# Optimization experiments

Hardware: AMD Instinct MI355X
Metric: run time of the kernel (lower is better)

The kernel has to match this reference:

```python
import jax, jax.numpy as jnp
import numpy as np

EMBED_DIM = 2048
NUM_EMBED = 1000
NUM_CLASSES = 1000
BS = 8192


def setup_inputs() -> dict:
    key = jax.random.key(0)
    ks = jax.random.split(key, 9)
    d = EMBED_DIM
    feat = jax.random.normal(ks[0], (BS, d), dtype=jnp.float32)
    # nn.Embedding weight init: uniform(0, 3)
    embeddings = jax.random.uniform(ks[1], (NUM_EMBED, d), dtype=jnp.float32, minval=0.0, maxval=3.0)
    # kaiming normal for square attention matrices
    std = float(np.sqrt(2.0 / d))
    Kw = jax.random.normal(ks[2], (d, d), dtype=jnp.float32) * std
    Qw = jax.random.normal(ks[3], (d, d), dtype=jnp.float32) * std
    Vw = jax.random.normal(ks[4], (d, d), dtype=jnp.float32) * std
    # fc_fuse: Linear(2d -> d); torch default uniform(-1/sqrt(fan_in), 1/sqrt(fan_in))
    b1 = 1.0 / np.sqrt(2 * d)
    fuse_w = jax.random.uniform(ks[5], (d, 2 * d), dtype=jnp.float32, minval=-b1, maxval=b1)
    fuse_b = jax.random.uniform(ks[6], (d,), dtype=jnp.float32, minval=-b1, maxval=b1)
    b2 = 1.0 / np.sqrt(d)
    fc_w = jax.random.uniform(ks[7], (NUM_CLASSES, d), dtype=jnp.float32, minval=-b2, maxval=b2)
    fc_b = jax.random.uniform(ks[8], (NUM_CLASSES,), dtype=jnp.float32, minval=-b2, maxval=b2)
    return {"feat": feat, "embeddings": embeddings, "Kw": Kw, "Qw": Qw, "Vw": Vw,
            "fuse_w": fuse_w, "fuse_b": fuse_b, "fc_w": fc_w, "fc_b": fc_b}


def _l2norm(x, axis=1, eps=1e-12):
    n = jnp.sqrt(jnp.sum(x * x, axis=axis, keepdims=True))
    return x / jnp.maximum(n, eps)


def reference(feat, embeddings, Kw, Qw, Vw, fuse_w, fuse_b, fc_w, fc_b):
    bs = feat.shape[0]
    # --- get_code_indices: normalize rows, pairwise sq-distance, argmin ---
    xn = _l2norm(feat)                       # [bs, d]
    wn = _l2norm(embeddings)                 # [N, d]
    distances = (jnp.sum(xn * xn, axis=1, keepdims=True)
                 + jnp.sum(wn * wn, axis=1)
                 - 2.0 * xn @ wn.T)          # [bs, N]
    idx = jnp.argmin(distances, axis=1)      # [bs]
    # quantize gathers from the UNnormalized table
    quantized = embeddings[idx]              # [bs, d]
    # --- tiny-sequence KQV attention over the 2-token 'sequence' ---
    fuse = jnp.stack([quantized, feat], axis=2)          # [bs, d, 2]
    K = jnp.einsum('ij,bjk->bik', Kw, fuse)              # [bs, d, 2]
    Q = jnp.einsum('ij,bjk->bik', Qw, fuse)              # [bs, d, 2]
    V = jnp.einsum('ij,bjk->bik', Vw, fuse)              # [bs, d, 2]
    scores = jnp.einsum('bdk,bdl->bkl', K, Q)            # K^T Q, [bs, 2, 2]
    # eval-path softmax over dim=1 (no sqrt(2) scaling)
    A = jax.nn.softmax(scores, axis=1)                   # [bs, 2, 2]
    out = jnp.einsum('bdk,bkl->bdl', V, A)               # [bs, d, 2]
    flat = jnp.transpose(out, (0, 2, 1)).reshape(bs, -1) # [bs, 2d]
    h = jax.nn.relu(flat @ fuse_w.T + fuse_b)            # [bs, d]
    pred = h @ fc_w.T + fc_b                             # [bs, num_classes]
    return (quantized, pred, idx)
```

## Files before the change

kernel.cpp:

```cpp
#include <hip/hip_runtime.h>
#include <cstdint>
#include <cstddef>


typedef __bf16 bf16;
typedef __bf16 bf16x8 __attribute__((ext_vector_type(8)));
typedef float  f32x4  __attribute__((ext_vector_type(4)));

#define TO_AS1(p) ((__attribute__((address_space(1))) void*)(uintptr_t)(p))
#define TO_AS3(p) ((__attribute__((address_space(3))) void*)(uintptr_t)(p))

enum { EPI_DIST = 1, EPI_SCORES = 2, EPI_BIAS = 4 };

__device__ __forceinline__ void stage_b(const bf16* __restrict__ src, char* lds,
                                        int rbase, int ld, int k0, int clamp,
                                        int tid) {
  const int wb = tid & ~63, lane = tid & 63;
#pragma unroll
  for (int it = 0; it < 4; ++it) {
    const int chunk = it * 256 + wb + lane;
    const int rloc = chunk >> 3;
    int row = rbase + rloc;
    if (row > clamp) row = clamp;
    const int sc = (chunk & 7) ^ (rloc & 7);
    const bf16* gp = src + (size_t)row * ld + k0 + sc * 8;
    __builtin_amdgcn_global_load_lds(TO_AS1(gp),
                                     TO_AS3(lds + (it * 256 + wb) * 16), 16, 0,
                                     0);
  }
}

__device__ __forceinline__ void stage_f(const float* __restrict__ src,
                                        char* lds, int rbase, int ld, int k0,
                                        int clamp, int tid) {
  const int wb = tid & ~63, lane = tid & 63;
#pragma unroll
  for (int it = 0; it < 8; ++it) {
    const int chunk = it * 256 + wb + lane;
    const int rloc = chunk >> 4;
    int row = rbase + rloc;
    if (row > clamp) row = clamp;
    const int sc = (chunk & 15) ^ (rloc & 7);
    const float* gp = src + (size_t)row * ld + k0 + sc * 4;
    __builtin_amdgcn_global_load_lds(TO_AS1(gp),
                                     TO_AS3(lds + (it * 256 + wb) * 16), 16, 0,
                                     0);
  }
}

__device__ __forceinline__ bf16x8 frag_b(const char* lds, int r, int koff) {
  const int cc = (koff >> 3) ^ (r & 7);
  return *(const bf16x8*)(lds + r * 128 + cc * 16);
}

__device__ __forceinline__ bf16x8 frag_f(const char* lds, int r, int koff) {
  const int c0 = koff >> 2;
  const f32x4 v0 = *(const f32x4*)(lds + r * 256 + ((c0 ^ (r & 7)) << 4));
  const f32x4 v1 =
      *(const f32x4*)(lds + r * 256 + (((c0 + 1) ^ (r & 7)) << 4));
  bf16x8 h;
#pragma unroll
  for (int t = 0; t < 4; ++t) { h[t] = (bf16)v0[t]; h[4 + t] = (bf16)v1[t]; }
  return h;
}

template <int EPI, bool TRIPLE, int MINW>
__global__ __launch_bounds__(256, MINW) void gemm_nt(
    const bf16* __restrict__ AH, const bf16* __restrict__ AL,
    const bf16* __restrict__ BH, const bf16* __restrict__ BL,
    void* __restrict__ Cout, const float* __restrict__ bias,
    const float* __restrict__ qp, float* __restrict__ sA,
    const float* __restrict__ nx, const float* __restrict__ nw,
    const float* __restrict__ sw, float* __restrict__ Dmin,
    int* __restrict__ Darg, int K, int lda, int ldb, int ldc, int nclamp) {
  __shared__ __align__(16) char AsH[16384];
  __shared__ __align__(16) char BsH[16384];
  __shared__ __align__(16) char AsL[TRIPLE ? 16384 : 16];
  __shared__ __align__(16) char BsL[TRIPLE ? 16384 : 16];

  const int tid = threadIdx.x;
  const int wave = tid >> 6, lane = tid & 63;
  const int bm = blockIdx.x * 128, bn = blockIdx.y * 128;

  f32x4 acc[4][4] = {};

  const int fm = lane & 15;
  const int fk = (lane >> 4) * 8;
  const int wm = (wave >> 1) * 64;
  const int wn = (wave & 1) * 64;

  for (int k0 = 0; k0 < K; k0 += 64) {
    stage_b(AH, AsH, bm, lda, k0, 1 << 30, tid);
    stage_b(BH, BsH, bn, ldb, k0, nclamp, tid);
    if constexpr (TRIPLE) {
      stage_b(AL, AsL, bm, lda, k0, 1 << 30, tid);
      stage_b(BL, BsL, bn, ldb, k0, nclamp, tid);
    }
    __builtin_amdgcn_s_waitcnt(0);
    __syncthreads();
#pragma unroll
    for (int ks = 0; ks < 2; ++ks) {
      const int ko = ks * 32 + fk;
      bf16x8 ah[4], bh[4];
#pragma unroll
      for (int i = 0; i < 4; ++i) ah[i] = frag_b(AsH, wm + 16 * i + fm, ko);
#pragma unroll
      for (int j = 0; j < 4; ++j) bh[j] = frag_b(BsH, wn + 16 * j + fm, ko);
      if constexpr (TRIPLE) {
        bf16x8 al[4], bl[4];
#pragma unroll
        for (int i = 0; i < 4; ++i) al[i] = frag_b(AsL, wm + 16 * i + fm, ko);
#pragma unroll
        for (int j = 0; j < 4; ++j) bl[j] = frag_b(BsL, wn + 16 * j + fm, ko);
#pragma unroll
        for (int i = 0; i < 4; ++i)
#pragma unroll
          for (int j = 0; j < 4; ++j) {
            acc[i][j] = __builtin_amdgcn_mfma_f32_16x16x32_bf16(
                ah[i], bh[j], acc[i][j], 0, 0, 0);
            acc[i][j] = __builtin_amdgcn_mfma_f32_16x16x32_bf16(
                ah[i], bl[j], acc[i][j], 0, 0, 0);
            acc[i][j] = __builtin_amdgcn_mfma_f32_16x16x32_bf16(
                al[i], bh[j], acc[i][j], 0, 0, 0);
          }
      } else {
#pragma unroll
        for (int i = 0; i < 4; ++i)
#pragma unroll
          for (int j = 0; j < 4; ++j)
            acc[i][j] = __builtin_amdgcn_mfma_f32_16x16x32_bf16(
                ah[i], bh[j], acc[i][j], 0, 0, 0);
      }
    }
    __syncthreads();
  }

  const int r0 = (lane >> 4) * 4;

  if constexpr (EPI == EPI_DIST) {
    __shared__ float vred[256];
    __shared__ int ared[256];
    const float INF = 3.4e38f;
#pragma unroll
    for (int i = 0; i < 4; ++i) {
#pragma unroll
      for (int r = 0; r < 4; ++r) {
        const int rl = wm + 16 * i + r0 + r;
        const float rx = nx[bm + rl];
        float best = INF;
        int barg = 0;
#pragma unroll
        for (int j = 0; j < 4; ++j) {
          const int col = bn + wn + 16 * j + fm;
          if (col <= nclamp) {
            float s = sw[col] - 2.0f * acc[i][j][r] / (rx * nw[col]);
            if (s < best) { best = s; barg = col; }
          }
        }
#pragma unroll
        for (int o = 8; o >= 1; o >>= 1) {
          float ob = __shfl_xor(best, o, 64);
          int oa = __shfl_xor(barg, o, 64);
          if (ob < best || (ob == best && oa < barg)) { best = ob; barg = oa; }
        }
        if (fm == 0) {
          vred[rl * 2 + (wave & 1)] = best;
          ared[rl * 2 + (wave & 1)] = barg;
        }
      }
    }
    __syncthreads();
    if (tid < 128) {
      float v0 = vred[tid * 2], v1 = vred[tid * 2 + 1];
      int a0 = ared[tid * 2], a1 = ared[tid * 2 + 1];
      float bv = v0; int ba = a0;
      if (v1 < bv || (v1 == bv && a1 < ba)) { bv = v1; ba = a1; }
      Dmin[(size_t)(bm + tid) * 8 + blockIdx.y] = bv;
      Darg[(size_t)(bm + tid) * 8 + blockIdx.y] = ba;
    }
    return;
  }

  if constexpr (EPI == EPI_SCORES) {
#pragma unroll
    for (int i = 0; i < 4; ++i) {
#pragma unroll
      for (int r = 0; r < 4; ++r) {
        const int row = bm + wm + 16 * i + r0 + r;
        float pa = 0.f;
#pragma unroll
        for (int j = 0; j < 4; ++j) {
          const int col = bn + wn + 16 * j + fm;
          pa += qp[(size_t)row * 2048 + col] * acc[i][j][r];
        }
#pragma unroll
        for (int o = 8; o >= 1; o >>= 1) pa += __shfl_xor(pa, o, 64);
        if (fm == 0) atomicAdd(&sA[row], pa);
      }
    }
    return;
  }

#pragma unroll
  for (int i = 0; i < 4; ++i)
#pragma unroll
    for (int j = 0; j < 4; ++j) {
      const int col = bn + wn + 16 * j + fm;
#pragma unroll
      for (int r = 0; r < 4; ++r) {
        const int row = bm + wm + 16 * i + r0 + r;
        int bc = col <= nclamp ? col : nclamp;
        float v = acc[i][j][r] + bias[bc];
        if (col <= nclamp) ((float*)Cout)[(size_t)row * ldc + col] = v;
      }
    }
}

template <bool AF32, bool F32OUT, int MINW>
__global__ __launch_bounds__(256, MINW) void gemm4_nt(
    const void* a0, const void* a1, const void* a2, const void* a3,
    const bf16* b0, const bf16* b1, const bf16* b2, const bf16* b3, void* c0,
    void* c1, void* c2, void* c3, int K, int lda01, int lda23, int ldb,
    int ldc, int mclamp) {
  __shared__ __align__(16) char AsRaw[AF32 ? 32768 : 16384];
  __shared__ __align__(16) char BsRaw[16384];
  const int z = blockIdx.z;
  const void* A = z == 0 ? a0 : z == 1 ? a1 : z == 2 ? a2 : a3;
  const bf16* B = z == 0 ? b0 : z == 1 ? b1 : z == 2 ? b2 : b3;
  void* C = z == 0 ? c0 : z == 1 ? c1 : z == 2 ? c2 : c3;
  const int lda = (z < 2) ? lda01 : lda23;

  const int tid = threadIdx.x;
  const int wave = tid >> 6, lane = tid & 63;
  const int bm = blockIdx.x * 128, bn = blockIdx.y * 128;
  f32x4 acc[4][4] = {};
  const int fm = lane & 15, fk = (lane >> 4) * 8;
  const int wm = (wave >> 1) * 64, wn = (wave & 1) * 64;

  for (int k0 = 0; k0 < K; k0 += 64) {
    if constexpr (AF32)
      stage_f((const float*)A, AsRaw, bm, lda, k0, mclamp, tid);
    else
      stage_b((const bf16*)A, AsRaw, bm, lda, k0, mclamp, tid);
    stage_b(B, BsRaw, bn, ldb, k0, 1 << 30, tid);
    __builtin_amdgcn_s_waitcnt(0);
    __syncthreads();
#pragma unroll
    for (int ks = 0; ks < 2; ++ks) {
      const int ko = ks * 32 + fk;
      bf16x8 ah[4], bh[4];
#pragma unroll
      for (int i = 0; i < 4; ++i)
        ah[i] = AF32 ? frag_f(AsRaw, wm + 16 * i + fm, ko)
                     : frag_b(AsRaw, wm + 16 * i + fm, ko);
#pragma unroll
      for (int j = 0; j < 4; ++j) bh[j] = frag_b(BsRaw, wn + 16 * j + fm, ko);
#pragma unroll
      for (int i = 0; i < 4; ++i)
#pragma unroll
        for (int j = 0; j < 4; ++j)
          acc[i][j] = __builtin_amdgcn_mfma_f32_16x16x32_bf16(ah[i], bh[j],
                                                              acc[i][j], 0, 0, 0);
    }
    __syncthreads();
  }

  const int r0 = (lane >> 4) * 4;
#pragma unroll
  for (int i = 0; i < 4; ++i)
#pragma unroll
    for (int j = 0; j < 4; ++j) {
      const int col = bn + wn + 16 * j + fm;
#pragma unroll
      for (int r = 0; r < 4; ++r) {
        const int row = bm + wm + 16 * i + r0 + r;
        if (row <= mclamp) {
          if constexpr (F32OUT)
            ((float*)C)[(size_t)row * ldc + col] = acc[i][j][r];
          else
            ((bf16*)C)[(size_t)row * ldc + col] = (bf16)acc[i][j][r];
        }
      }
    }
}

__global__ __launch_bounds__(256, 2) void gemm_h(
    const float* __restrict__ A, const bf16* __restrict__ B1,
    const bf16* __restrict__ B2, bf16* __restrict__ H,
    const bf16* __restrict__ Z0, const float* __restrict__ Amat) {
  __shared__ __align__(16) char As[32768];
  __shared__ __align__(16) char Bs1[16384];
  __shared__ __align__(16) char Bs2[16384];
  const int tid = threadIdx.x;
  const int wave = tid >> 6, lane = tid & 63;
  const int bm = blockIdx.x * 128, bn = blockIdx.y * 128;
  f32x4 acc1[4][4] = {}, acc2[4][4] = {};
  const int fm = lane & 15, fk = (lane >> 4) * 8;
  const int wm = (wave >> 1) * 64, wn = (wave & 1) * 64;

  for (int k0 = 0; k0 < 2048; k0 += 64) {
    stage_f(A, As, bm, 2048, k0, 1 << 30, tid);
    stage_b(B1, Bs1, bn, 2048, k0, 1 << 30, tid);
    stage_b(B2, Bs2, bn, 2048, k0, 1 << 30, tid);
    __builtin_amdgcn_s_waitcnt(0);
    __syncthreads();
#pragma unroll
    for (int ks = 0; ks < 2; ++ks) {
      const int ko = ks * 32 + fk;
      bf16x8 ah[4], b1f[4], b2f[4];
#pragma unroll
      for (int i = 0; i < 4; ++i) ah[i] = frag_f(As, wm + 16 * i + fm, ko);
#pragma unroll
      for (int j = 0; j < 4; ++j) b1f[j] = frag_b(Bs1, wn + 16 * j + fm, ko);
#pragma unroll
      for (int j = 0; j < 4; ++j) b2f[j] = frag_b(Bs2, wn + 16 * j + fm, ko);
#pragma unroll
      for (int i = 0; i < 4; ++i)
#pragma unroll
        for (int j = 0; j < 4; ++j) {
          acc1[i][j] = __builtin_amdgcn_mfma_f32_16x16x32_bf16(
              ah[i], b1f[j], acc1[i][j], 0, 0, 0);
          acc2[i][j] = __builtin_amdgcn_mfma_f32_16x16x32_bf16(
              ah[i], b2f[j], acc2[i][j], 0, 0, 0);
        }
    }
    __syncthreads();
  }

  const int r0 = (lane >> 4) * 4;
#pragma unroll
  for (int i = 0; i < 4; ++i)
#pragma unroll
    for (int r = 0; r < 4; ++r) {
      const int row = bm + wm + 16 * i + r0 + r;
      const f32x4 a = *(const f32x4*)(Amat + (size_t)row * 4);
#pragma unroll
      for (int j = 0; j < 4; ++j) {
        const int col = bn + wn + 16 * j + fm;
        float z = (float)Z0[(size_t)row * 2048 + col];
        float v = a[1] * acc1[i][j][r] + a[3] * acc2[i][j][r] + z;
        H[(size_t)row * 2048 + col] = (bf16)(v > 0.f ? v : 0.f);
      }
    }
}

__global__ void zero_k(float* __restrict__ p) {
  p[blockIdx.x * 256 + threadIdx.x] = 0.f;
}

__global__ void cvt_k(const float* __restrict__ src, bf16* __restrict__ hi,
                      bf16* __restrict__ lo) {
  const size_t i = ((size_t)blockIdx.x * 256 + threadIdx.x) * 8;
  f32x4 a = *(const f32x4*)(src + i);
  f32x4 b = *(const f32x4*)(src + i + 4);
  bf16x8 h;
#pragma unroll
  for (int t = 0; t < 4; ++t) { h[t] = (bf16)a[t]; h[4 + t] = (bf16)b[t]; }
  *(bf16x8*)(hi + i) = h;
  if (lo) {
    bf16x8 l;
#pragma unroll
    for (int t = 0; t < 4; ++t) {
      l[t] = (bf16)(a[t] - (float)h[t]);
      l[4 + t] = (bf16)(b[t] - (float)h[4 + t]);
    }
    *(bf16x8*)(lo + i) = l;
  }
}

__global__ void zgather_k(const int* __restrict__ idxb,
                          const float* __restrict__ Amat,
                          const float* __restrict__ T1,
                          const float* __restrict__ T2,
                          const float* __restrict__ fb,
                          bf16* __restrict__ Z0) {
  const int b = blockIdx.x;
  const int ix = idxb[b];
  const float a00 = Amat[(size_t)b * 4 + 0];
  const float a01 = Amat[(size_t)b * 4 + 2];
  const int i = threadIdx.x * 8;
  const float* t1p = T1 + (size_t)ix * 2048 + i;
  const float* t2p = T2 + (size_t)ix * 2048 + i;
  f32x4 t1a = *(const f32x4*)t1p, t1b = *(const f32x4*)(t1p + 4);
  f32x4 t2a = *(const f32x4*)t2p, t2b = *(const f32x4*)(t2p + 4);
  f32x4 fba = *(const f32x4*)(fb + i), fbb = *(const f32x4*)(fb + i + 4);
  bf16x8 z;
#pragma unroll
  for (int t = 0; t < 4; ++t) {
    z[t] = (bf16)(a00 * t1a[t] + a01 * t2a[t] + fba[t]);
    z[4 + t] = (bf16)(a00 * t1b[t] + a01 * t2b[t] + fbb[t]);
  }
  *(bf16x8*)(Z0 + (size_t)b * 2048 + i) = z;
}

__global__ void transpose3_k(const float* __restrict__ Kw,
                             const float* __restrict__ Qw,
                             const float* __restrict__ Vw,
                             bf16* __restrict__ KwT, bf16* __restrict__ QwT,
                             bf16* __restrict__ VwT) {
  __shared__ float tile[64][65];
  const int z = blockIdx.z;
  const float* src = z == 0 ? Kw : z == 1 ? Qw : Vw;
  bf16* dst = z == 0 ? KwT : z == 1 ? QwT : VwT;
  const int bx = blockIdx.x * 64, by = blockIdx.y * 64;
  const int tx = threadIdx.x & 63, ty = threadIdx.x >> 6;
  for (int r = ty; r < 64; r += 4)
    tile[r][tx] = src[(size_t)(by + r) * 2048 + bx + tx];
  __syncthreads();
  for (int r = ty; r < 64; r += 4)
    dst[(size_t)(bx + r) * 2048 + by + tx] = (bf16)tile[tx][r];
}

__device__ __forceinline__ float block_sum(float v, float* sbuf) {
#pragma unroll
  for (int o = 32; o > 0; o >>= 1) v += __shfl_down(v, o, 64);
  const int wave = threadIdx.x >> 6, lane = threadIdx.x & 63;
  if (lane == 0) sbuf[wave] = v;
  __syncthreads();
  float r = sbuf[0] + sbuf[1] + sbuf[2] + sbuf[3];
  __syncthreads();
  return r;
}

__global__ void feat_norm_k(const float* __restrict__ x, float* __restrict__ nx) {
  __shared__ float sbuf[4];
  const float* row = x + (size_t)blockIdx.x * 2048;
  f32x4 a = *(const f32x4*)(row + threadIdx.x * 8);
  f32x4 b = *(const f32x4*)(row + threadIdx.x * 8 + 4);
  float s = 0.f;
#pragma unroll
  for (int t = 0; t < 4; ++t) s += a[t] * a[t] + b[t] * b[t];
  float tot = block_sum(s, sbuf);
  if (threadIdx.x == 0) nx[blockIdx.x] = fmaxf(sqrtf(tot), 1e-12f);
}

__global__ void emb_norm_k(const float* __restrict__ w, float* __restrict__ nw,
                           float* __restrict__ sw) {
  __shared__ float sbuf[4];
  const float* row = w + (size_t)blockIdx.x * 2048;
  f32x4 a = *(const f32x4*)(row + threadIdx.x * 8);
  f32x4 b = *(const f32x4*)(row + threadIdx.x * 8 + 4);
  float s = 0.f;
#pragma unroll
  for (int t = 0; t < 4; ++t) s += a[t] * a[t] + b[t] * b[t];
  float n = fmaxf(sqrtf(block_sum(s, sbuf)), 1e-12f);
  float s2 = 0.f;
#pragma unroll
  for (int t = 0; t < 4; ++t) {
    float va = a[t] / n, vb = b[t] / n;
    s2 += va * va + vb * vb;
  }
  float tot2 = block_sum(s2, sbuf);
  if (threadIdx.x == 0) { nw[blockIdx.x] = n; sw[blockIdx.x] = tot2; }
}

__global__ void idx_sel_k(const float* __restrict__ Dmin,
                          const int* __restrict__ Darg, int* __restrict__ idxb,
                          float* __restrict__ out_idx) {
  const int b = blockIdx.x * 256 + threadIdx.x;
  float best = 3.4e38f;
  int idx = 0;
  bool found = false;
  for (int t = 0; t < 8; ++t) {
    float v = Dmin[(size_t)b * 8 + t];
    int a = Darg[(size_t)b * 8 + t];
    if (!(v == v) || a < 0 || a >= 1000) continue;
    if (!found || v < best || (v == best && a < idx)) {
      best = v; idx = a; found = true;
    }
  }
  if (idx < 0) idx = 0;
  if (idx > 999) idx = 999;
  idxb[b] = idx;
  out_idx[b] = (float)idx;
}

__global__ void t00_k(const float* __restrict__ EG, const float* __restrict__ emb,
                      float* __restrict__ t00) {
  __shared__ float sbuf[4];
  const int i = blockIdx.x, t = threadIdx.x;
  const float* a = EG + (size_t)i * 2048;
  const float* e = emb + (size_t)i * 2048;
  f32x4 va = *(const f32x4*)(a + t * 8), vb = *(const f32x4*)(a + t * 8 + 4);
  f32x4 ea = *(const f32x4*)(e + t * 8), eb = *(const f32x4*)(e + t * 8 + 4);
  float s = 0.f;
#pragma unroll
  for (int u = 0; u < 4; ++u) s += va[u] * ea[u] + vb[u] * eb[u];
  float r = block_sum(s, sbuf);
  if (t == 0) t00[i] = r;
}

__global__ void score_gather_k(const float* __restrict__ feat,
                               const float* __restrict__ EG,
                               const float* __restrict__ EGT,
                               const float* __restrict__ t00,
                               const int* __restrict__ idxb,
                               float* __restrict__ s00, float* __restrict__ s10,
                               float* __restrict__ s01) {
  __shared__ float sbuf[4];
  const int b = blockIdx.x, t = threadIdx.x;
  const int ix = idxb[b];
  const float* f = feat + (size_t)b * 2048;
  const float* eg = EG + (size_t)ix * 2048;
  const float* eh = EGT + (size_t)ix * 2048;
  f32x4 fa = *(const f32x4*)(f + t * 8), fb2 = *(const f32x4*)(f + t * 8 + 4);
  f32x4 ga = *(const f32x4*)(eg + t * 8), gb = *(const f32x4*)(eg + t * 8 + 4);
  f32x4 ha = *(const f32x4*)(eh + t * 8), hb = *(const f32x4*)(eh + t * 8 + 4);
  float d01 = 0.f, d10 = 0.f;
#pragma unroll
  for (int u = 0; u < 4; ++u) {
    d01 += fa[u] * ga[u] + fb2[u] * gb[u];
    d10 += fa[u] * ha[u] + fb2[u] * hb[u];
  }
  float r01 = block_sum(d01, sbuf);
  float r10 = block_sum(d10, sbuf);
  if (t == 0) { s01[b] = r01; s10[b] = r10; s00[b] = t00[ix]; }
}

__global__ void scores_final_k(const float* __restrict__ s00p,
                               const float* __restrict__ s10p,
                               const float* __restrict__ s01p,
                               const float* __restrict__ s11p,
                               float* __restrict__ Amat) {
  const int b = blockIdx.x * 256 + threadIdx.x;
  float t00 = s00p[b], t10 = s10p[b], t01 = s01p[b], t11 = s11p[b];
  float m0 = fmaxf(t00, t10), m1 = fmaxf(t01, t11);
  float e00 = expf(t00 - m0), e10 = expf(t10 - m0);
  float e01 = expf(t01 - m1), e11 = expf(t11 - m1);
  float d0 = e00 + e10, d1 = e01 + e11;
  float* Ab = Amat + (size_t)b * 4;
  Ab[0] = e00 / d0; Ab[1] = e10 / d0; Ab[2] = e01 / d1; Ab[3] = e11 / d1;
}

__global__ void gather_q_k(const int* __restrict__ idxb,
                           const float* __restrict__ emb,
                           float* __restrict__ outq) {
  const int b = blockIdx.x;
  const int ix = idxb[b];
  const f32x4* src = (const f32x4*)(emb + (size_t)ix * 2048);
  f32x4* dst = (f32x4*)(outq + (size_t)b * 2048);
  dst[threadIdx.x] = src[threadIdx.x];
  dst[threadIdx.x + 256] = src[threadIdx.x + 256];
}

extern "C" void kernel_launch(void* const* d_in, const int* in_sizes, int n_in,
                              void* d_out, int out_size, void* d_ws,
                              size_t ws_size, hipStream_t stream) {
  const float* feat = (const float*)d_in[0];
  const float* emb = (const float*)d_in[1];
  const float* Kw = (const float*)d_in[2];
  const float* Qw = (const float*)d_in[3];
  const float* Vw = (const float*)d_in[4];
  const float* fuse_w = (const float*)d_in[5];
  const float* fuse_b = (const float*)d_in[6];
  const float* fc_w = (const float*)d_in[7];
  const float* fc_b = (const float*)d_in[8];

  float* out_q = (float*)d_out;
  float* out_pred = out_q + (size_t)8192 * 2048;
  float* out_idx = out_pred + (size_t)8192 * 1000;

  char* ws = (char*)d_ws;
  const size_t MiB = 1024 * 1024;
  float* nx = (float*)(ws + 0);
  float* nw = (float*)(ws + 32768);
  float* swp = (float*)(ws + 36864);
  float* t00 = (float*)(ws + 40960);
  int* idxb = (int*)(ws + 45056);
  float* s00 = (float*)(ws + 81920);
  float* s10 = (float*)(ws + 114688);
  float* s01 = (float*)(ws + 147456);
  float* s11 = (float*)(ws + 180224);
  float* Amat = (float*)(ws + 212992);
  float* Dmin = (float*)(ws + 360448);
  int* Darg = (int*)(ws + 622592);
  bf16* G = (bf16*)(ws + 1 * MiB);
  bf16* GT = (bf16*)(ws + 9 * MiB);
  bf16* M1 = (bf16*)(ws + 17 * MiB);
  bf16* M2 = (bf16*)(ws + 25 * MiB);
  bf16* embH = (bf16*)(ws + 9 * MiB);
  bf16* embL = (bf16*)(ws + 9 * MiB + 4096000);
  bf16* fc_wB = (bf16*)(ws + 17 * MiB);

  char* oq = (char*)out_q;
  bf16* KwT = (bf16*)oq;
  bf16* QwT = (bf16*)(oq + 8 * MiB);
  bf16* VwT = (bf16*)(oq + 16 * MiB);
  bf16* fuse_wB = (bf16*)(oq + 24 * MiB);
  bf16* featH = (bf16*)oq;
  bf16* featL = (bf16*)(oq + 32 * MiB);
  bf16* Z0 = (bf16*)(oq + 32 * MiB);
  bf16* Hbuf = (bf16*)oq;

  float* EG = out_pred;
  float* EGT = out_pred + (size_t)2048 * 1000;
  float* T1 = out_pred + (size_t)4096 * 1000;
  float* T2 = out_pred + (size_t)6144 * 1000;

  feat_norm_k<<<8192, 256, 0, stream>>>(feat, nx);
  emb_norm_k<<<1000, 256, 0, stream>>>(emb, nw, swp);
  zero_k<<<32, 256, 0, stream>>>(s11);
  transpose3_k<<<dim3(32, 32, 3), 256, 0, stream>>>(Kw, Qw, Vw, KwT, QwT, VwT);
  cvt_k<<<4096, 256, 0, stream>>>(fuse_w, fuse_wB, nullptr);

  gemm4_nt<false, false, 4><<<dim3(16, 16, 4), 256, 0, stream>>>(
      KwT, QwT, fuse_wB, fuse_wB + 2048, QwT, KwT, VwT, VwT, G, GT, M1, M2,
      2048, 2048, 4096, 2048, 2048, 1 << 30);

  gemm4_nt<true, true, 3><<<dim3(8, 16, 4), 256, 0, stream>>>(
      emb, emb, emb, emb, GT, G, M1, M2, EG, EGT, T1, T2, 2048, 2048, 2048,
      2048, 2048, 999);
  t00_k<<<1000, 256, 0, stream>>>(EG, emb, t00);

  cvt_k<<<1000, 256, 0, stream>>>(emb, embH, embL);
  cvt_k<<<8192, 256, 0, stream>>>(feat, featH, featL);

  gemm_nt<EPI_DIST, true, 2><<<dim3(64, 8), 256, 0, stream>>>(
      featH, featL, embH, embL, nullptr, nullptr, nullptr, nullptr, nx, nw,
      swp, Dmin, Darg, 2048, 2048, 2048, 0, 999);
  idx_sel_k<<<32, 256, 0, stream>>>(Dmin, Darg, idxb, out_idx);
  score_gather_k<<<8192, 256, 0, stream>>>(feat, EG, EGT, t00, idxb, s00, s10,
                                           s01);

  gemm_nt<EPI_SCORES, false, 4><<<dim3(64, 16), 256, 0, stream>>>(
      featH, nullptr, G, nullptr, nullptr, nullptr, feat, s11, nullptr,
      nullptr, nullptr, nullptr, nullptr, 2048, 2048, 2048, 0, 2047);
  scores_final_k<<<32, 256, 0, stream>>>(s00, s10, s01, s11, Amat);

  zgather_k<<<8192, 256, 0, stream>>>(idxb, Amat, T1, T2, fuse_b, Z0);

  gemm_h<<<dim3(64, 16), 256, 0, stream>>>(feat, M1, M2, Hbuf, Z0, Amat);

  cvt_k<<<1000, 256, 0, stream>>>(fc_w, fc_wB, nullptr);

  gemm_nt<EPI_BIAS, false, 4><<<dim3(64, 8), 256, 0, stream>>>(
      Hbuf, nullptr, fc_wB, nullptr, out_pred, fc_b, nullptr, nullptr, nullptr,
      nullptr, nullptr, nullptr, nullptr, 2048, 2048, 2048, 1000, 999);

  gather_q_k<<<8192, 256, 0, stream>>>(idxb, emb, out_q);
}
```

Baseline: 811.9 us.

## Fuse norms into bf16 conversion, derive GT by transpose, feed gemm_h bf16 features

```diff
diff --git a/kernel.cpp b/kernel.cpp
--- a/kernel.cpp
+++ b/kernel.cpp
@@ -220,7 +220,7 @@
 __global__ __launch_bounds__(256, MINW) void gemm4_nt(
     const void* a0, const void* a1, const void* a2, const void* a3,
     const bf16* b0, const bf16* b1, const bf16* b2, const bf16* b3, void* c0,
-    void* c1, void* c2, void* c3, int K, int lda01, int lda23, int ldb,
+    void* c1, void* c2, void* c3, int K, int lda0, int ldaR, int ldb,
     int ldc, int mclamp) {
   __shared__ __align__(16) char AsRaw[AF32 ? 32768 : 16384];
   __shared__ __align__(16) char BsRaw[16384];
@@ -228,7 +228,7 @@
   const void* A = z == 0 ? a0 : z == 1 ? a1 : z == 2 ? a2 : a3;
   const bf16* B = z == 0 ? b0 : z == 1 ? b1 : z == 2 ? b2 : b3;
   void* C = z == 0 ? c0 : z == 1 ? c1 : z == 2 ? c2 : c3;
-  const int lda = (z < 2) ? lda01 : lda23;
+  const int lda = (z == 0) ? lda0 : ldaR;
 
   const int tid = threadIdx.x;
   const int wave = tid >> 6, lane = tid & 63;
@@ -284,11 +284,11 @@
     }
 }
 
-__global__ __launch_bounds__(256, 2) void gemm_h(
-    const float* __restrict__ A, const bf16* __restrict__ B1,
+__global__ __launch_bounds__(256, 3) void gemm_h(
+    const bf16* __restrict__ A, const bf16* __restrict__ B1,
     const bf16* __restrict__ B2, bf16* __restrict__ H,
     const bf16* __restrict__ Z0, const float* __restrict__ Amat) {
-  __shared__ __align__(16) char As[32768];
+  __shared__ __align__(16) char As[16384];
   __shared__ __align__(16) char Bs1[16384];
   __shared__ __align__(16) char Bs2[16384];
   const int tid = threadIdx.x;
@@ -299,7 +299,7 @@
   const int wm = (wave >> 1) * 64, wn = (wave & 1) * 64;
 
   for (int k0 = 0; k0 < 2048; k0 += 64) {
-    stage_f(A, As, bm, 2048, k0, 1 << 30, tid);
+    stage_b(A, As, bm, 2048, k0, 1 << 30, tid);
     stage_b(B1, Bs1, bn, 2048, k0, 1 << 30, tid);
     stage_b(B2, Bs2, bn, 2048, k0, 1 << 30, tid);
     __builtin_amdgcn_s_waitcnt(0);
@@ -309,7 +309,7 @@
       const int ko = ks * 32 + fk;
       bf16x8 ah[4], b1f[4], b2f[4];
 #pragma unroll
-      for (int i = 0; i < 4; ++i) ah[i] = frag_f(As, wm + 16 * i + fm, ko);
+      for (int i = 0; i < 4; ++i) ah[i] = frag_b(As, wm + 16 * i + fm, ko);
 #pragma unroll
       for (int j = 0; j < 4; ++j) b1f[j] = frag_b(Bs1, wn + 16 * j + fm, ko);
 #pragma unroll
@@ -348,8 +348,7 @@
   p[blockIdx.x * 256 + threadIdx.x] = 0.f;
 }
 
-__global__ void cvt_k(const float* __restrict__ src, bf16* __restrict__ hi,
-                      bf16* __restrict__ lo) {
+__global__ void cvt_k(const float* __restrict__ src, bf16* __restrict__ hi) {
   const size_t i = ((size_t)blockIdx.x * 256 + threadIdx.x) * 8;
   f32x4 a = *(const f32x4*)(src + i);
   f32x4 b = *(const f32x4*)(src + i + 4);
@@ -357,15 +356,67 @@
 #pragma unroll
   for (int t = 0; t < 4; ++t) { h[t] = (bf16)a[t]; h[4 + t] = (bf16)b[t]; }
   *(bf16x8*)(hi + i) = h;
-  if (lo) {
-    bf16x8 l;
-#pragma unroll
-    for (int t = 0; t < 4; ++t) {
-      l[t] = (bf16)(a[t] - (float)h[t]);
-      l[4 + t] = (bf16)(b[t] - (float)h[4 + t]);
-    }
-    *(bf16x8*)(lo + i) = l;
-  }
+}
+
+__device__ __forceinline__ float block_sum(float v, float* sbuf) {
+#pragma unroll
+  for (int o = 32; o > 0; o >>= 1) v += __shfl_down(v, o, 64);
+  const int wave = threadIdx.x >> 6, lane = threadIdx.x & 63;
+  if (lane == 0) sbuf[wave] = v;
+  __syncthreads();
+  float r = sbuf[0] + sbuf[1] + sbuf[2] + sbuf[3];
+  __syncthreads();
+  return r;
+}
+
+__global__ void featcvt_k(const float* __restrict__ x, bf16* __restrict__ H,
+                          bf16* __restrict__ L, float* __restrict__ nx) {
+  __shared__ float sbuf[4];
+  const size_t base = (size_t)blockIdx.x * 2048 + threadIdx.x * 8;
+  f32x4 a = *(const f32x4*)(x + base);
+  f32x4 b = *(const f32x4*)(x + base + 4);
+  bf16x8 h, l;
+  float s = 0.f;
+#pragma unroll
+  for (int t = 0; t < 4; ++t) {
+    h[t] = (bf16)a[t]; h[4 + t] = (bf16)b[t];
+    l[t] = (bf16)(a[t] - (float)h[t]);
+    l[4 + t] = (bf16)(b[t] - (float)h[4 + t]);
+    s += a[t] * a[t] + b[t] * b[t];
+  }
+  *(bf16x8*)(H + base) = h;
+  *(bf16x8*)(L + base) = l;
+  float tot = block_sum(s, sbuf);
+  if (threadIdx.x == 0) nx[blockIdx.x] = fmaxf(sqrtf(tot), 1e-12f);
+}
+
+__global__ void embcvt_k(const float* __restrict__ x, bf16* __restrict__ H,
+                         bf16* __restrict__ L, float* __restrict__ nw,
+                         float* __restrict__ sw) {
+  __shared__ float sbuf[4];
+  const size_t base = (size_t)blockIdx.x * 2048 + threadIdx.x * 8;
+  f32x4 a = *(const f32x4*)(x + base);
+  f32x4 b = *(const f32x4*)(x + base + 4);
+  bf16x8 h, l;
+  float s = 0.f;
+#pragma unroll
+  for (int t = 0; t < 4; ++t) {
+    h[t] = (bf16)a[t]; h[4 + t] = (bf16)b[t];
+    l[t] = (bf16)(a[t] - (float)h[t]);
+    l[4 + t] = (bf16)(b[t] - (float)h[4 + t]);
+    s += a[t] * a[t] + b[t] * b[t];
+  }
+  *(bf16x8*)(H + base) = h;
+  *(bf16x8*)(L + base) = l;
+  float n = fmaxf(sqrtf(block_sum(s, sbuf)), 1e-12f);
+  float s2 = 0.f;
+#pragma unroll
+  for (int t = 0; t < 4; ++t) {
+    float va = a[t] / n, vb = b[t] / n;
+    s2 += va * va + vb * vb;
+  }
+  float tot2 = block_sum(s2, sbuf);
+  if (threadIdx.x == 0) { nw[blockIdx.x] = n; sw[blockIdx.x] = tot2; }
 }
 
 __global__ void zgather_k(const int* __restrict__ idxb,
@@ -411,47 +462,16 @@
     dst[(size_t)(bx + r) * 2048 + by + tx] = (bf16)tile[tx][r];
 }
 
-__device__ __forceinline__ float block_sum(float v, float* sbuf) {
-#pragma unroll
-  for (int o = 32; o > 0; o >>= 1) v += __shfl_down(v, o, 64);
-  const int wave = threadIdx.x >> 6, lane = threadIdx.x & 63;
-  if (lane == 0) sbuf[wave] = v;
+__global__ void transpose_g_k(const bf16* __restrict__ src,
+                              bf16* __restrict__ dst) {
+  __shared__ bf16 tile[64][65];
+  const int bx = blockIdx.x * 64, by = blockIdx.y * 64;
+  const int tx = threadIdx.x & 63, ty = threadIdx.x >> 6;
+  for (int r = ty; r < 64; r += 4)
+    tile[r][tx] = src[(size_t)(by + r) * 2048 + bx + tx];
   __syncthreads();
-  float r = sbuf[0] + sbuf[1] + sbuf[2] + sbuf[3];
-  __syncthreads();
-  return r;
-}
-
-__global__ void feat_norm_k(const float* __restrict__ x, float* __restrict__ nx) {
-  __shared__ float sbuf[4];
-  const float* row = x + (size_t)blockIdx.x * 2048;
-  f32x4 a = *(const f32x4*)(row + threadIdx.x * 8);
-  f32x4 b = *(const f32x4*)(row + threadIdx.x * 8 + 4);
-  float s = 0.f;
-#pragma unroll
-  for (int t = 0; t < 4; ++t) s += a[t] * a[t] + b[t] * b[t];
-  float tot = block_sum(s, sbuf);
-  if (threadIdx.x == 0) nx[blockIdx.x] = fmaxf(sqrtf(tot), 1e-12f);
-}
-
-__global__ void emb_norm_k(const float* __restrict__ w, float* __restrict__ nw,
-                           float* __restrict__ sw) {
-  __shared__ float sbuf[4];
-  const float* row = w + (size_t)blockIdx.x * 2048;
-  f32x4 a = *(const f32x4*)(row + threadIdx.x * 8);
-  f32x4 b = *(const f32x4*)(row + threadIdx.x * 8 + 4);
-  float s = 0.f;
-#pragma unroll
-  for (int t = 0; t < 4; ++t) s += a[t] * a[t] + b[t] * b[t];
-  float n = fmaxf(sqrtf(block_sum(s, sbuf)), 1e-12f);
-  float s2 = 0.f;
-#pragma unroll
-  for (int t = 0; t < 4; ++t) {
-    float va = a[t] / n, vb = b[t] / n;
-    s2 += va * va + vb * vb;
-  }
-  float tot2 = block_sum(s2, sbuf);
-  if (threadIdx.x == 0) { nw[blockIdx.x] = n; sw[blockIdx.x] = tot2; }
+  for (int r = ty; r < 64; r += 4)
+    dst[(size_t)(bx + r) * 2048 + by + tx] = tile[tx][r];
 }
 
 __global__ void idx_sel_k(const float* __restrict__ Dmin,
@@ -590,30 +610,30 @@
   bf16* featH = (bf16*)oq;
   bf16* featL = (bf16*)(oq + 32 * MiB);
   bf16* Z0 = (bf16*)(oq + 32 * MiB);
-  bf16* Hbuf = (bf16*)oq;
+  bf16* Hbuf = Z0;
 
   float* EG = out_pred;
   float* EGT = out_pred + (size_t)2048 * 1000;
   float* T1 = out_pred + (size_t)4096 * 1000;
   float* T2 = out_pred + (size_t)6144 * 1000;
 
-  feat_norm_k<<<8192, 256, 0, stream>>>(feat, nx);
-  emb_norm_k<<<1000, 256, 0, stream>>>(emb, nw, swp);
   zero_k<<<32, 256, 0, stream>>>(s11);
   transpose3_k<<<dim3(32, 32, 3), 256, 0, stream>>>(Kw, Qw, Vw, KwT, QwT, VwT);
-  cvt_k<<<4096, 256, 0, stream>>>(fuse_w, fuse_wB, nullptr);
-
-  gemm4_nt<false, false, 4><<<dim3(16, 16, 4), 256, 0, stream>>>(
-      KwT, QwT, fuse_wB, fuse_wB + 2048, QwT, KwT, VwT, VwT, G, GT, M1, M2,
-      2048, 2048, 4096, 2048, 2048, 1 << 30);
+  cvt_k<<<4096, 256, 0, stream>>>(fuse_w, fuse_wB);
+
+  gemm4_nt<false, false, 4><<<dim3(16, 16, 3), 256, 0, stream>>>(
+      KwT, fuse_wB, fuse_wB + 2048, nullptr, QwT, VwT, VwT, nullptr, G, M1, M2,
+      nullptr, 2048, 2048, 4096, 2048, 2048, 1 << 30);
+
+  transpose_g_k<<<dim3(32, 32), 256, 0, stream>>>(G, GT);
 
   gemm4_nt<true, true, 3><<<dim3(8, 16, 4), 256, 0, stream>>>(
       emb, emb, emb, emb, GT, G, M1, M2, EG, EGT, T1, T2, 2048, 2048, 2048,
       2048, 2048, 999);
   t00_k<<<1000, 256, 0, stream>>>(EG, emb, t00);
 
-  cvt_k<<<1000, 256, 0, stream>>>(emb, embH, embL);
-  cvt_k<<<8192, 256, 0, stream>>>(feat, featH, featL);
+  featcvt_k<<<8192, 256, 0, stream>>>(feat, featH, featL, nx);
+  embcvt_k<<<1000, 256, 0, stream>>>(emb, embH, embL, nw, swp);
 
   gemm_nt<EPI_DIST, true, 2><<<dim3(64, 8), 256, 0, stream>>>(
       featH, featL, embH, embL, nullptr, nullptr, nullptr, nullptr, nx, nw,
@@ -629,9 +649,9 @@
 
   zgather_k<<<8192, 256, 0, stream>>>(idxb, Amat, T1, T2, fuse_b, Z0);
 
-  gemm_h<<<dim3(64, 16), 256, 0, stream>>>(feat, M1, M2, Hbuf, Z0, Amat);
-
-  cvt_k<<<1000, 256, 0, stream>>>(fc_w, fc_wB, nullptr);
+  gemm_h<<<dim3(64, 16), 256, 0, stream>>>(featH, M1, M2, Hbuf, Z0, Amat);
+
+  cvt_k<<<1000, 256, 0, stream>>>(fc_w, fc_wB);
 
   gemm_nt<EPI_BIAS, false, 4><<<dim3(64, 8), 256, 0, stream>>>(
       Hbuf, nullptr, fc_wB, nullptr, out_pred, fc_b, nullptr, nullptr, nullptr,
```

Measured after the change: 1.092 ms. 34.5% more time.
